# Performance work log

Hardware: AMD Instinct MI355X
Metric: run time of the kernel (lower is better)

The kernel has to match this reference:

```python
import jax, jax.numpy as jnp
import numpy as np


def _init_relative_position_index(window_size: int) -> np.ndarray:
    coords = np.stack(np.meshgrid(np.arange(window_size), np.arange(window_size), indexing='ij'))
    coords_flatten = coords.reshape(2, -1)  # [2, wh*ww]
    rel = coords_flatten[:, :, None] - coords_flatten[:, None, :]  # [2, N, N]
    rel = rel.transpose(1, 2, 0).copy()
    rel[:, :, 0] += window_size - 1
    rel[:, :, 1] += window_size - 1
    rel[:, :, 0] *= 2 * window_size - 1
    return rel.sum(-1)  # [N, N] int


def setup_inputs() -> dict:
    B_, N, C, H, WH, NW = 2048, 49, 512, 16, 7, 64
    key = jax.random.key(0)
    ks = jax.random.split(key, 6)
    x = jax.random.normal(ks[0], (B_, N, C), dtype=jnp.float32)
    qkv_w = jax.random.normal(ks[1], (3 * C, C), dtype=jnp.float32) * 0.02
    qkv_b = jax.random.normal(ks[2], (3 * C,), dtype=jnp.float32) * 0.02
    rp_bias_table = jax.random.normal(ks[3], ((2 * WH - 1) ** 2, H), dtype=jnp.float32) * 0.02
    out_w = jax.random.normal(ks[4], (C, C), dtype=jnp.float32) * 0.02
    out_b = jax.random.normal(ks[5], (C,), dtype=jnp.float32) * 0.02
    rp_index = jnp.asarray(_init_relative_position_index(WH), dtype=jnp.int32)
    mask = jnp.zeros((NW, N, N), dtype=jnp.float32)  # 0/-inf shifted-window mask
    return {"x": x, "qkv_w": qkv_w, "qkv_b": qkv_b, "rp_index": rp_index,
            "rp_bias_table": rp_bias_table, "out_w": out_w, "out_b": out_b,
            "mask": mask, "nw": NW}


def reference(x, qkv_w, qkv_b, rp_index, rp_bias_table, out_w, out_b, mask, nw):
    B_, N, C = x.shape
    h = rp_bias_table.shape[1]
    dh = C // h
    scale = float(dh) ** -0.5

    # QKV projection; weight layout is (h dh 3) x C per the module's note.
    qkv = x @ qkv_w.T + qkv_b                      # [B_, N, 3C]
    qkv = qkv.reshape(B_, N, h, dh, 3)             # [B_, N, h, dh, 3]
    q = qkv[..., 0].transpose(0, 2, 1, 3)          # [B_, h, N, dh]
    k = qkv[..., 1].transpose(0, 2, 1, 3)
    v = qkv[..., 2].transpose(0, 2, 1, 3)

    attn = jnp.einsum('bhnd,bhmd->bhnm', q * scale, k)  # [B_, h, N, N]

    # gather relative position bias: [N*N] -> [N, N, h] -> [h, N, N]
    pb = rp_bias_table[rp_index.reshape(-1)].reshape(N, N, h).transpose(2, 0, 1)
    # NOTE: original adds the bias TWICE (attn += pb; attn += pb[None]); replicate.
    attn = attn + pb[None]
    attn = attn + pb[None]

    nW = mask.shape[0]
    attn = attn.reshape(B_ // nW, nW, h, N, N) + mask[None, :, None]
    attn = attn.reshape(B_, h, N, N)
    attn = jax.nn.softmax(attn, axis=-1)
    # attn_drop = proj_drop = 0.0 -> dropout is identity

    out = jnp.einsum('bhnm,bhmd->bhnd', attn, v)   # [B_, h, N, dh]
    out = out.transpose(0, 2, 1, 3).reshape(B_, N, h * dh)
    out = out @ out_w.T + out_b
    return out
```

## Files before the change

kernel.cpp:

```cpp
#include <hip/hip_runtime.h>
#include <hip/hip_bf16.h>
#include <stdint.h>

typedef short s16x8 __attribute__((ext_vector_type(8)));
typedef float f32x4 __attribute__((ext_vector_type(4)));

#define H_ 16
#define DH 32
#define NTOK 49
#define CDIM 512
#define SCALE 0.17677669529663687f

typedef const __attribute__((address_space(1))) uint32_t* gas_ptr;
typedef __attribute__((address_space(3))) uint32_t* las_ptr;
#define GLL16(g, l) __builtin_amdgcn_global_load_lds((gas_ptr)(g), (las_ptr)(l), 16, 0, 0)

__device__ __forceinline__ short f2bf(float f){
  union { float f; uint32_t u; } v; v.f = f;
  uint32_t r = v.u + 0x7fffu + ((v.u >> 16) & 1u);
  return (short)(r >> 16);
}

__device__ __forceinline__ s16x8 pack8(float4 a, float4 b){
  s16x8 r;
  r[0]=f2bf(a.x); r[1]=f2bf(a.y); r[2]=f2bf(a.z); r[3]=f2bf(a.w);
  r[4]=f2bf(b.x); r[5]=f2bf(b.y); r[6]=f2bf(b.z); r[7]=f2bf(b.w);
  return r;
}

__global__ void prep_wq_kernel(const float* __restrict__ w, const float* __restrict__ b,
                               short* __restrict__ wq, float* __restrict__ pb)
{
  int t = blockIdx.x*256 + threadIdx.x;
  int jp = t >> 6, kg = t & 63;
  int s = jp >> 9, h = (jp >> 5) & 15, d = jp & 31;
  int srow = h*96 + d*3 + s;
  float fac = (s == 0) ? SCALE : 1.0f;
  const float* wr = w + (size_t)srow*CDIM + kg*8;
  float4 a = *(const float4*)wr;
  float4 c = *(const float4*)(wr+4);
  a.x*=fac; a.y*=fac; a.z*=fac; a.w*=fac;
  c.x*=fac; c.y*=fac; c.z*=fac; c.w*=fac;
  ((s16x8*)(wq + (size_t)jp*CDIM))[kg] = pack8(a,c);
  if (kg == 0) pb[jp] = b[srow]*fac;
}

__global__ void prep_wo_kernel(const float* __restrict__ w, short* __restrict__ wo)
{
  int t = blockIdx.x*256 + threadIdx.x;
  int j = t >> 6, kg = t & 63;
  const float* wr = w + (size_t)j*CDIM + kg*8;
  float4 a = *(const float4*)wr;
  float4 c = *(const float4*)(wr+4);
  ((s16x8*)(wo + (size_t)j*CDIM))[kg] = pack8(a,c);
}

__global__ void bias2_kernel(const int* __restrict__ idx, const float* __restrict__ tab,
                             float* __restrict__ b2)
{
  int i = blockIdx.x*256 + threadIdx.x;
  if (i < H_*2401){
    int h = i / 2401, rc = i - h*2401;
    b2[i] = 2.0f * tab[idx[rc]*H_ + h];
  }
}

__global__ void cvt_kernel(const float* __restrict__ src, short* __restrict__ dst, int n8)
{
  int i = blockIdx.x*blockDim.x + threadIdx.x;
  int stride = gridDim.x*blockDim.x;
  for (; i < n8; i += stride){
    float4 a = ((const float4*)src)[2*i];
    float4 b = ((const float4*)src)[2*i+1];
    ((s16x8*)dst)[i] = pack8(a,b);
  }
}

template<int EPI>
__global__ __launch_bounds__(256)
void gemm128(const short* __restrict__ A, const short* __restrict__ Bm,
             const float* __restrict__ pb,
             short* __restrict__ Q, short* __restrict__ Kd, short* __restrict__ V,
             float* __restrict__ outF, int ntiles, int b0)
{
  __shared__ __align__(16) short As[128*64];
  __shared__ __align__(16) short Bs[128*64];
  const int tid = threadIdx.x, w = tid >> 6, l = tid & 63;
  const int mt = blockIdx.x / ntiles, jt = blockIdx.x % ntiles;
  const int wr = w >> 1, wc = w & 1, lg = l >> 4, lc = l & 15;

  const int srow = w*8 + (l >> 3);
  const int kb = (l & 7) * 16;
  const char* ga = (const char*)A  + ((size_t)(mt*128 + srow))*1024 + kb;
  const char* gb = (const char*)Bm + ((size_t)(jt*128 + srow))*1024 + kb;

  f32x4 acc[4][4];
  #pragma unroll
  for (int i=0;i<4;++i)
    #pragma unroll
    for (int j=0;j<4;++j) acc[i][j] = (f32x4){0.f,0.f,0.f,0.f};

  for (int kt=0; kt<8; ++kt){
    const char* gak = ga + kt*128;
    const char* gbk = gb + kt*128;
    #pragma unroll
    for (int i=0;i<4;++i){
      GLL16(gak + i*32768, As + i*2048 + w*512);
      GLL16(gbk + i*32768, Bs + i*2048 + w*512);
    }
    __syncthreads();
    #pragma unroll
    for (int kk=0; kk<2; ++kk){
      s16x8 af[4], bf_[4];
      #pragma unroll
      for (int i=0;i<4;++i) af[i]  = *(const s16x8*)&As[(wr*64 + i*16 + lc)*64 + kk*32 + lg*8];
      #pragma unroll
      for (int j=0;j<4;++j) bf_[j] = *(const s16x8*)&Bs[(wc*64 + j*16 + lc)*64 + kk*32 + lg*8];
      #pragma unroll
      for (int i=0;i<4;++i)
        #pragma unroll
        for (int j=0;j<4;++j)
          acc[i][j] = __builtin_amdgcn_mfma_f32_16x16x32_bf16(af[i], bf_[j], acc[i][j], 0,0,0);
    }
    __syncthreads();
  }

  const int cb = jt*128 + wc*64;
  if (EPI == 0){
    const int s_sel = cb >> 9;
    short* dst = (s_sel==0) ? Q : (s_sel==1 ? Kd : V);
    float bv[4]; int hj[4], dj[4];
    #pragma unroll
    for (int j=0;j<4;++j){
      int cc = cb + j*16 + lc;
      bv[j] = pb[cc];
      hj[j] = (cc >> 5) & 15;
      dj[j] = cc & 31;
    }
    #pragma unroll
    for (int i=0;i<4;++i){
      #pragma unroll
      for (int r=0;r<4;++r){
        int grow = mt*128 + wr*64 + i*16 + lg*4 + r;
        int bl = grow / 49;
        int n  = grow - bl*49;
        #pragma unroll
        for (int j=0;j<4;++j)
          dst[(((size_t)bl*H_ + hj[j])*NTOK + n)*DH + dj[j]] = f2bf(acc[i][j][r] + bv[j]);
      }
    }
  } else {
    float bv[4];
    #pragma unroll
    for (int j=0;j<4;++j) bv[j] = pb[cb + j*16 + lc];
    #pragma unroll
    for (int i=0;i<4;++i){
      #pragma unroll
      for (int r=0;r<4;++r){
        int grow = mt*128 + wr*64 + i*16 + lg*4 + r;
        size_t o = ((size_t)(b0*NTOK) + grow)*CDIM + cb;
        #pragma unroll
        for (int j=0;j<4;++j)
          outF[o + j*16 + lc] = acc[i][j][r] + bv[j];
      }
    }
  }
}

__global__ __launch_bounds__(256)
void attn_kernel(const short* __restrict__ Q, const short* __restrict__ Kt,
                 const short* __restrict__ V, const float* __restrict__ bias2,
                 const float* __restrict__ mask, short* __restrict__ AO,
                 int b0, int nW)
{
  __shared__ __align__(16) short P[4][64][72];
  const int tid = threadIdx.x, wv = tid >> 6, lane = tid & 63;
  const int lg = lane >> 4, lc = lane & 15;
  const int pair = blockIdx.x*4 + wv;
  const int bl = pair >> 4, h = pair & 15;
  const short* q = Q  + ((size_t)bl*H_ + h)*NTOK*DH;
  const short* k = Kt + ((size_t)bl*H_ + h)*NTOK*DH;
  const short* v = V  + ((size_t)bl*H_ + h)*NTOK*DH;

  s16x8 qa[4], kb[4];
  #pragma unroll
  for (int t=0;t<4;++t){
    int r = t*16 + lc; if (r > 48) r = 48;
    qa[t] = *(const s16x8*)(q + r*DH + lg*8);
    kb[t] = *(const s16x8*)(k + r*DH + lg*8);
  }
  f32x4 S[4][4];
  #pragma unroll
  for (int i=0;i<4;++i)
    #pragma unroll
    for (int j=0;j<4;++j) S[i][j] = (f32x4){0.f,0.f,0.f,0.f};
  #pragma unroll
  for (int i=0;i<4;++i)
    #pragma unroll
    for (int j=0;j<4;++j)
      S[i][j] = __builtin_amdgcn_mfma_f32_16x16x32_bf16(qa[i], kb[j], S[i][j], 0,0,0);

  const float* bb = bias2 + (size_t)h*2401;
  const float* mm = mask + (size_t)((b0 + bl) % nW)*2401;

  float rinv[4][4];
  #pragma unroll
  for (int i=0;i<4;++i){
    #pragma unroll
    for (int r=0;r<4;++r){
      int row = i*16 + lg*4 + r;
      float mx = -3.0e38f;
      #pragma unroll
      for (int j=0;j<4;++j){
        int col = j*16 + lc;
        float sv = S[i][j][r];
        if (row < 49 && col < 49) sv += bb[row*49+col] + mm[row*49+col];
        else sv = -1.0e30f;
        S[i][j][r] = sv;
        mx = fmaxf(mx, sv);
      }
      #pragma unroll
      for (int off=1; off<16; off<<=1) mx = fmaxf(mx, __shfl_xor(mx, off, 64));
      float sum = 0.f;
      #pragma unroll
      for (int j=0;j<4;++j){
        float e = __expf(S[i][j][r] - mx);
        S[i][j][r] = e;
        sum += e;
      }
      #pragma unroll
      for (int off=1; off<16; off<<=1) sum += __shfl_xor(sum, off, 64);
      rinv[i][r] = 1.0f / sum;
    }
  }

  #pragma unroll
  for (int i=0;i<4;++i)
    #pragma unroll
    for (int j=0;j<4;++j)
      #pragma unroll
      for (int r=0;r<4;++r)
        P[wv][i*16 + lg*4 + r][j*16 + lc] = f2bf(S[i][j][r]);

  s16x8 vb[2][2];
  #pragma unroll
  for (int kt=0;kt<2;++kt)
    #pragma unroll
    for (int nt=0;nt<2;++nt){
      s16x8 t;
      #pragma unroll
      for (int e=0;e<8;++e){
        int kk = kt*32 + lg*8 + e; if (kk > 48) kk = 48;
        t[e] = v[kk*DH + nt*16 + lc];
      }
      vb[kt][nt] = t;
    }
  f32x4 O[4][2];
  #pragma unroll
  for (int i=0;i<4;++i){ O[i][0] = (f32x4){0.f,0.f,0.f,0.f}; O[i][1] = (f32x4){0.f,0.f,0.f,0.f}; }
  #pragma unroll
  for (int i=0;i<4;++i){
    #pragma unroll
    for (int kt=0;kt<2;++kt){
      s16x8 pa = *(const s16x8*)&P[wv][i*16 + lc][kt*32 + lg*8];
      #pragma unroll
      for (int nt=0;nt<2;++nt)
        O[i][nt] = __builtin_amdgcn_mfma_f32_16x16x32_bf16(pa, vb[kt][nt], O[i][nt], 0,0,0);
    }
  }
  #pragma unroll
  for (int i=0;i<4;++i)
    #pragma unroll
    for (int r=0;r<4;++r){
      int row = i*16 + lg*4 + r;
      if (row < 49){
        size_t o = ((size_t)bl*NTOK + row)*CDIM + h*DH;
        float rv = rinv[i][r];
        AO[o + lc]      = f2bf(O[i][0][r]*rv);
        AO[o + 16 + lc] = f2bf(O[i][1][r]*rv);
      }
    }
}

extern "C" void kernel_launch(void* const* d_in, const int* in_sizes, int n_in,
                              void* d_out, int out_size, void* d_ws, size_t ws_size,
                              hipStream_t stream)
{
  const float* x      = (const float*)d_in[0];
  const float* qkv_w  = (const float*)d_in[1];
  const float* qkv_b  = (const float*)d_in[2];
  const int*   rp_idx = (const int*)d_in[3];
  const float* rp_tab = (const float*)d_in[4];
  const float* out_w  = (const float*)d_in[5];
  const float* out_b  = (const float*)d_in[6];
  const float* mask   = (const float*)d_in[7];
  const int nW = in_sizes[7] / (NTOK*NTOK);
  float* out = (float*)d_out;

  char* base = (char*)d_ws;
  size_t off = 0;
  auto alloc = [&](size_t bytes)->char*{
    char* p = base + off;
    off = (off + bytes + 255) & ~(size_t)255;
    return p;
  };
  float* b2  = (float*)alloc((size_t)H_*2401*4);
  short* wq  = (short*)alloc((size_t)1536*CDIM*2);
  float* pbq = (float*)alloc(1536*4);
  short* wo  = (short*)alloc((size_t)CDIM*CDIM*2);

  int CB = 512;
  while (CB > 128){
    size_t need = off + 5*(size_t)CB*50176;
    if (need <= ws_size) break;
    CB >>= 1;
  }
  short* xb = (short*)alloc((size_t)CB*50176);
  short* Q  = (short*)alloc((size_t)CB*50176);
  short* K  = (short*)alloc((size_t)CB*50176);
  short* V  = (short*)alloc((size_t)CB*50176);
  short* AO = (short*)alloc((size_t)CB*50176);

  hipLaunchKernelGGL(bias2_kernel, dim3((H_*2401 + 255)/256), dim3(256), 0, stream,
                     rp_idx, rp_tab, b2);
  hipLaunchKernelGGL(prep_wq_kernel, dim3(1536*64/256), dim3(256), 0, stream,
                     qkv_w, qkv_b, wq, pbq);
  hipLaunchKernelGGL(prep_wo_kernel, dim3(512*64/256), dim3(256), 0, stream,
                     out_w, wo);

  const int nchunk = 2048 / CB;
  const int mtiles = CB*NTOK/128;
  const int n8 = CB*3136;
  for (int c=0; c<nchunk; ++c){
    int b0 = c*CB;
    hipLaunchKernelGGL(cvt_kernel, dim3(2048), dim3(256), 0, stream,
                       x + (size_t)b0*NTOK*CDIM, xb, n8);
    hipLaunchKernelGGL((gemm128<0>), dim3(mtiles*12), dim3(256), 0, stream,
                       xb, wq, pbq, Q, K, V, (float*)nullptr, 12, b0);
    hipLaunchKernelGGL(attn_kernel, dim3(CB*4), dim3(256), 0, stream,
                       Q, K, V, b2, mask, AO, b0, nW);
    hipLaunchKernelGGL((gemm128<1>), dim3(mtiles*4), dim3(256), 0, stream,
                       AO, wo, out_b, (short*)nullptr, (short*)nullptr, (short*)nullptr,
                       out, 4, b0);
  }
}
```

Before: 605.2 us.

## Double-buffer GEMM LDS loads, swizzle LDS and XCD mapping, pre-fuse bias with mask

The GEMM now double-buffers its global-to-LDS loads so the next K tile streams in while MFMAs run. It also XOR-swizzles the LDS layout to avoid bank conflicts, remaps workgroups across XCDs for L2 locality, and raises wave priority around the MFMA block. Separately, the doubled relative-position bias and the window mask are combined once into a per-window, per-head table, so attention does one load per element instead of two. The bf16 conversion now uses the compiler cast. The changes cost twice the GEMM LDS footprint and a larger bias table of nW*H*2401 floats.

Result: faster. 575.9 us (-4.9%).

```diff
diff --git a/kernel.cpp b/kernel.cpp
--- a/kernel.cpp
+++ b/kernel.cpp
@@ -16,9 +16,9 @@
 #define GLL16(g, l) __builtin_amdgcn_global_load_lds((gas_ptr)(g), (las_ptr)(l), 16, 0, 0)
 
 __device__ __forceinline__ short f2bf(float f){
-  union { float f; uint32_t u; } v; v.f = f;
-  uint32_t r = v.u + 0x7fffu + ((v.u >> 16) & 1u);
-  return (short)(r >> 16);
+  union { __bf16 h; short s; } u;
+  u.h = (__bf16)f;
+  return u.s;
 }
 
 __device__ __forceinline__ s16x8 pack8(float4 a, float4 b){
@@ -26,6 +26,12 @@
   r[0]=f2bf(a.x); r[1]=f2bf(a.y); r[2]=f2bf(a.z); r[3]=f2bf(a.w);
   r[4]=f2bf(b.x); r[5]=f2bf(b.y); r[6]=f2bf(b.z); r[7]=f2bf(b.w);
   return r;
+}
+
+__device__ __forceinline__ int xcd_swz(int orig, int nwg){
+  int q = nwg >> 3, r = nwg & 7;
+  int x = orig & 7, idx = orig >> 3;
+  return (x < r ? x*(q+1) : r*(q+1) + (x - r)*q) + idx;
 }
 
 __global__ void prep_wq_kernel(const float* __restrict__ w, const float* __restrict__ b,
@@ -55,14 +61,15 @@
   ((s16x8*)(wo + (size_t)j*CDIM))[kg] = pack8(a,c);
 }
 
-__global__ void bias2_kernel(const int* __restrict__ idx, const float* __restrict__ tab,
-                             float* __restrict__ b2)
-{
-  int i = blockIdx.x*256 + threadIdx.x;
-  if (i < H_*2401){
-    int h = i / 2401, rc = i - h*2401;
-    b2[i] = 2.0f * tab[idx[rc]*H_ + h];
-  }
+__global__ void prep_bm_kernel(const int* __restrict__ idx, const float* __restrict__ tab,
+                               const float* __restrict__ mask, float* __restrict__ bm)
+{
+  int wh = blockIdx.x;
+  int w = wh >> 4, h = wh & 15;
+  const float* mw = mask + (size_t)w*2401;
+  float* o = bm + (size_t)wh*2401;
+  for (int i = threadIdx.x; i < 2401; i += 256)
+    o[i] = mw[i] + 2.0f*tab[idx[i]*H_ + h];
 }
 
 __global__ void cvt_kernel(const float* __restrict__ src, short* __restrict__ dst, int n8)
@@ -81,18 +88,19 @@
 void gemm128(const short* __restrict__ A, const short* __restrict__ Bm,
              const float* __restrict__ pb,
              short* __restrict__ Q, short* __restrict__ Kd, short* __restrict__ V,
-             float* __restrict__ outF, int ntiles, int b0)
-{
-  __shared__ __align__(16) short As[128*64];
-  __shared__ __align__(16) short Bs[128*64];
+             float* __restrict__ outF, int ntiles, int nwg, int b0)
+{
+  __shared__ __align__(16) short As[2][8192];
+  __shared__ __align__(16) short Bs[2][8192];
   const int tid = threadIdx.x, w = tid >> 6, l = tid & 63;
-  const int mt = blockIdx.x / ntiles, jt = blockIdx.x % ntiles;
+  const int wg = xcd_swz(blockIdx.x, nwg);
+  const int mt = wg / ntiles, jt = wg % ntiles;
   const int wr = w >> 1, wc = w & 1, lg = l >> 4, lc = l & 15;
 
   const int srow = w*8 + (l >> 3);
-  const int kb = (l & 7) * 16;
-  const char* ga = (const char*)A  + ((size_t)(mt*128 + srow))*1024 + kb;
-  const char* gb = (const char*)Bm + ((size_t)(jt*128 + srow))*1024 + kb;
+  const int sbyte = ((l & 7) ^ (l >> 3)) << 4;
+  const char* gA = (const char*)A  + ((size_t)(mt*128 + srow))*1024 + sbyte;
+  const char* gB = (const char*)Bm + ((size_t)(jt*128 + srow))*1024 + sbyte;
 
   f32x4 acc[4][4];
   #pragma unroll
@@ -100,29 +108,46 @@
     #pragma unroll
     for (int j=0;j<4;++j) acc[i][j] = (f32x4){0.f,0.f,0.f,0.f};
 
+  #pragma unroll
+  for (int i=0;i<4;++i){
+    GLL16(gA + i*32768, (char*)As[0] + i*4096 + w*1024);
+    GLL16(gB + i*32768, (char*)Bs[0] + i*4096 + w*1024);
+  }
+  __syncthreads();
+
+  int buf = 0;
   for (int kt=0; kt<8; ++kt){
-    const char* gak = ga + kt*128;
-    const char* gbk = gb + kt*128;
-    #pragma unroll
-    for (int i=0;i<4;++i){
-      GLL16(gak + i*32768, As + i*2048 + w*512);
-      GLL16(gbk + i*32768, Bs + i*2048 + w*512);
-    }
-    __syncthreads();
+    if (kt < 7){
+      const char* ga2 = gA + (kt+1)*128;
+      const char* gb2 = gB + (kt+1)*128;
+      #pragma unroll
+      for (int i=0;i<4;++i){
+        GLL16(ga2 + i*32768, (char*)As[buf^1] + i*4096 + w*1024);
+        GLL16(gb2 + i*32768, (char*)Bs[buf^1] + i*4096 + w*1024);
+      }
+    }
+    const char* pA = (const char*)As[buf];
+    const char* pB = (const char*)Bs[buf];
     #pragma unroll
     for (int kk=0; kk<2; ++kk){
+      const int kbyte = (kk*64 + lg*16) ^ ((lc & 7) << 4);
       s16x8 af[4], bf_[4];
       #pragma unroll
-      for (int i=0;i<4;++i) af[i]  = *(const s16x8*)&As[(wr*64 + i*16 + lc)*64 + kk*32 + lg*8];
-      #pragma unroll
-      for (int j=0;j<4;++j) bf_[j] = *(const s16x8*)&Bs[(wc*64 + j*16 + lc)*64 + kk*32 + lg*8];
+      for (int i=0;i<4;++i)
+        af[i]  = *(const s16x8*)(pA + (wr*64 + i*16 + lc)*128 + kbyte);
+      #pragma unroll
+      for (int j=0;j<4;++j)
+        bf_[j] = *(const s16x8*)(pB + (wc*64 + j*16 + lc)*128 + kbyte);
+      __builtin_amdgcn_s_setprio(1);
       #pragma unroll
       for (int i=0;i<4;++i)
         #pragma unroll
         for (int j=0;j<4;++j)
           acc[i][j] = __builtin_amdgcn_mfma_f32_16x16x32_bf16(af[i], bf_[j], acc[i][j], 0,0,0);
+      __builtin_amdgcn_s_setprio(0);
     }
     __syncthreads();
+    buf ^= 1;
   }
 
   const int cb = jt*128 + wc*64;
@@ -169,9 +194,8 @@
 
 __global__ __launch_bounds__(256)
 void attn_kernel(const short* __restrict__ Q, const short* __restrict__ Kt,
-                 const short* __restrict__ V, const float* __restrict__ bias2,
-                 const float* __restrict__ mask, short* __restrict__ AO,
-                 int b0, int nW)
+                 const short* __restrict__ V, const float* __restrict__ bm,
+                 short* __restrict__ AO, int b0, int nW)
 {
   __shared__ __align__(16) short P[4][64][72];
   const int tid = threadIdx.x, wv = tid >> 6, lane = tid & 63;
@@ -200,8 +224,8 @@
     for (int j=0;j<4;++j)
       S[i][j] = __builtin_amdgcn_mfma_f32_16x16x32_bf16(qa[i], kb[j], S[i][j], 0,0,0);
 
-  const float* bb = bias2 + (size_t)h*2401;
-  const float* mm = mask + (size_t)((b0 + bl) % nW)*2401;
+  const int widx = (b0 + bl) % nW;
+  const float* bmh = bm + ((size_t)widx*H_ + h)*2401;
 
   float rinv[4][4];
   #pragma unroll
@@ -214,7 +238,7 @@
       for (int j=0;j<4;++j){
         int col = j*16 + lc;
         float sv = S[i][j][r];
-        if (row < 49 && col < 49) sv += bb[row*49+col] + mm[row*49+col];
+        if (row < 49 && col < 49) sv += bmh[row*49+col];
         else sv = -1.0e30f;
         S[i][j][r] = sv;
         mx = fmaxf(mx, sv);
@@ -304,7 +328,7 @@
     off = (off + bytes + 255) & ~(size_t)255;
     return p;
   };
-  float* b2  = (float*)alloc((size_t)H_*2401*4);
+  float* bm  = (float*)alloc((size_t)nW*H_*2401*4);
   short* wq  = (short*)alloc((size_t)1536*CDIM*2);
   float* pbq = (float*)alloc(1536*4);
   short* wo  = (short*)alloc((size_t)CDIM*CDIM*2);
@@ -321,8 +345,8 @@
   short* V  = (short*)alloc((size_t)CB*50176);
   short* AO = (short*)alloc((size_t)CB*50176);
 
-  hipLaunchKernelGGL(bias2_kernel, dim3((H_*2401 + 255)/256), dim3(256), 0, stream,
-                     rp_idx, rp_tab, b2);
+  hipLaunchKernelGGL(prep_bm_kernel, dim3(nW*H_), dim3(256), 0, stream,
+                     rp_idx, rp_tab, mask, bm);
   hipLaunchKernelGGL(prep_wq_kernel, dim3(1536*64/256), dim3(256), 0, stream,
                      qkv_w, qkv_b, wq, pbq);
   hipLaunchKernelGGL(prep_wo_kernel, dim3(512*64/256), dim3(256), 0, stream,
@@ -336,11 +360,11 @@
     hipLaunchKernelGGL(cvt_kernel, dim3(2048), dim3(256), 0, stream,
                        x + (size_t)b0*NTOK*CDIM, xb, n8);
     hipLaunchKernelGGL((gemm128<0>), dim3(mtiles*12), dim3(256), 0, stream,
-                       xb, wq, pbq, Q, K, V, (float*)nullptr, 12, b0);
+                       xb, wq, pbq, Q, K, V, (float*)nullptr, 12, mtiles*12, b0);
     hipLaunchKernelGGL(attn_kernel, dim3(CB*4), dim3(256), 0, stream,
-                       Q, K, V, b2, mask, AO, b0, nW);
+                       Q, K, V, bm, AO, b0, nW);
     hipLaunchKernelGGL((gemm128<1>), dim3(mtiles*4), dim3(256), 0, stream,
                        AO, wo, out_b, (short*)nullptr, (short*)nullptr, (short*)nullptr,
-                       out, 4, b0);
-  }
-}
+                       out, 4, mtiles*4, b0);
+  }
+}
```
